# Kernel optimization log

Measured on AMD Instinct MI355X. Metric: run time of the kernel, lower is better.

Reference implementation:

```python
import jax, jax.numpy as jnp
import numpy as np

N_HEAD = 16

def setup_inputs() -> dict:
    key = jax.random.key(0)
    k1, k2, k3 = jax.random.split(key, 3)
    B, T, E = 4, 2048, 1024
    x = jax.random.normal(k1, (B, T, E), dtype=jnp.float32)
    w_attn = jax.random.normal(k2, (4 * E, E), dtype=jnp.float32) * (1.0 / np.sqrt(E))
    b_attn = jax.random.normal(k3, (4 * E,), dtype=jnp.float32) * 0.02
    return {"x": x, "w_attn": w_attn, "b_attn": b_attn}

def reference(x, w_attn, b_attn):
    B, T, C = x.shape
    H = N_HEAD
    D = C // H  # head_dim
    qkv = x @ w_attn.T + b_attn                      # [B,T,4C]
    q, k, v = qkv[..., :C], qkv[..., C:2*C], qkv[..., 2*C:3*C]  # 4th chunk unused
    q = q.reshape(B, T, H, D).transpose(0, 2, 1, 3)  # [B,H,T,D]
    k = k.reshape(B, T, H, D).transpose(0, 2, 1, 3)
    v = v.reshape(B, T, H, D).transpose(0, 2, 1, 3)
    scale = 1.0 / np.sqrt(D)
    attn = jnp.einsum('bhqd,bhkd->bhqk', q, k) * scale  # [B,H,T,T]
    causal = jnp.tril(jnp.ones((T, T), dtype=bool))
    attn = jnp.where(causal[None, None], attn, -jnp.inf)
    attn = jax.nn.softmax(attn, axis=-1)
    y = jnp.einsum('bhqk,bhkd->bhqd', attn, v)       # [B,H,T,D]
    return y.transpose(0, 2, 1, 3).reshape(B, T, C)
```

## Files before the change

kernel.cpp:

```cpp
#include <hip/hip_runtime.h>
#include <math.h>


using short8 = __attribute__((ext_vector_type(8))) short;
using f32x4  = __attribute__((ext_vector_type(4))) float;

__device__ __forceinline__ ushort f2bf(float f) {
    union { float f; unsigned u; } x{f};
    unsigned r = x.u + 0x7fffu + ((x.u >> 16) & 1u);
    return (ushort)(r >> 16);
}
__device__ __forceinline__ unsigned pack_bf16_ru(float a, float b) {
    union { float f; unsigned u; } x{a}, y{b};
    return __builtin_amdgcn_perm(y.u + 0x8000u, x.u + 0x8000u, 0x07060302u);
}

__device__ __forceinline__ void gload_lds16(const void* g, void* l) {
    __builtin_amdgcn_global_load_lds(
        (const __attribute__((address_space(1))) void*)g,
        (__attribute__((address_space(3))) void*)l, 16, 0, 0);
}

__global__ void cvt_all(const float* __restrict__ x, const float* __restrict__ w,
                        ushort* __restrict__ xb, ushort* __restrict__ wb) {
    int i = blockIdx.x * blockDim.x + threadIdx.x;
    const float* src; ushort* dst; int j;
    if (i < 2097152) { src = x; dst = xb; j = i; }
    else             { src = w; dst = wb; j = i - 2097152; if (j >= 786432) return; }
    float4 v = ((const float4*)src)[j];
    ushort4 o;
    o.x = f2bf(v.x); o.y = f2bf(v.y); o.z = f2bf(v.z); o.w = f2bf(v.w);
    ((ushort4*)dst)[j] = o;
}

__global__ __launch_bounds__(256) void qkv_gemm(
    const ushort* __restrict__ A, const ushort* __restrict__ W,
    const float* __restrict__ bias,
    ushort* __restrict__ Qo, ushort* __restrict__ Ko, ushort* __restrict__ Vt)
{
    __shared__ ushort As[128 * 64];
    __shared__ ushort Ws[128 * 64];
    const int id = (int)blockIdx.x;
    const int xcd = id & 7, s = id >> 3;
    const int bm = xcd * 8 + (s & 7);
    const int bn = s >> 3;
    const int tid = threadIdx.x;
    const int wave = tid >> 6, lane = tid & 63;
    const int quad = lane >> 4, l16 = lane & 15, l7 = l16 & 7;
    const int wm = (wave >> 1) * 64, wn = (wave & 1) * 64;

    const ushort* Abase = A + (size_t)(bm * 128) * 1024;
    const ushort* Wbase = W + (size_t)(bn * 128) * 1024;

    f32x4 acc[4][4];
#pragma unroll
    for (int i = 0; i < 4; i++)
#pragma unroll
        for (int j = 0; j < 4; j++) acc[i][j] = (f32x4){0.f, 0.f, 0.f, 0.f};

    for (int k0 = 0; k0 < 1024; k0 += 64) {
        __syncthreads();
#pragma unroll
        for (int j = 0; j < 4; j++) {
            const int rb = wave * 32 + j * 8;
            const int r  = rb + (lane >> 3);
            const int cc = (lane & 7) ^ (r & 7);
            gload_lds16(Abase + (size_t)r * 1024 + k0 + cc * 8, &As[rb * 64]);
            gload_lds16(Wbase + (size_t)r * 1024 + k0 + cc * 8, &Ws[rb * 64]);
        }
        __syncthreads();
        short8 af[4][2], wf[4][2];
#pragma unroll
        for (int t = 0; t < 4; t++)
#pragma unroll
            for (int kg = 0; kg < 2; kg++) {
                const int pc = ((kg * 4 + quad) ^ l7) * 8;
                af[t][kg] = *(const short8*)&As[(wm + t * 16 + l16) * 64 + pc];
                wf[t][kg] = *(const short8*)&Ws[(wn + t * 16 + l16) * 64 + pc];
            }
#pragma unroll
        for (int kg = 0; kg < 2; kg++)
#pragma unroll
            for (int tm = 0; tm < 4; tm++)
#pragma unroll
                for (int tn = 0; tn < 4; tn++)
                    acc[tm][tn] = __builtin_amdgcn_mfma_f32_16x16x32_bf16(af[tm][kg], wf[tn][kg], acc[tm][tn], 0, 0, 0);
    }

    const float SCALE_Q = 0.125f * 1.4426950408889634f;
#pragma unroll
    for (int tn = 0; tn < 4; tn++) {
        const int n = bn * 128 + wn + tn * 16 + l16;
        const float bv = bias[n];
#pragma unroll
        for (int tm = 0; tm < 4; tm++) {
            const int m0 = bm * 128 + wm + tm * 16 + quad * 4;
            const int b0 = m0 >> 11, t0 = m0 & 2047;
            if (n < 1024) {
                const int h = n >> 6, d = n & 63;
#pragma unroll
                for (int r = 0; r < 4; r++)
                    Qo[((size_t)(b0 * 16 + h) * 2048 + t0 + r) * 64 + d] = f2bf((acc[tm][tn][r] + bv) * SCALE_Q);
            } else if (n < 2048) {
                const int c = n - 1024, h = c >> 6, d = c & 63;
#pragma unroll
                for (int r = 0; r < 4; r++)
                    Ko[((size_t)(b0 * 16 + h) * 2048 + t0 + r) * 64 + d] = f2bf(acc[tm][tn][r] + bv);
            } else {
                const int c = n - 2048, h = c >> 6, d = c & 63;
                uint2 pk;
                pk.x = pack_bf16_ru(acc[tm][tn][0] + bv, acc[tm][tn][1] + bv);
                pk.y = pack_bf16_ru(acc[tm][tn][2] + bv, acc[tm][tn][3] + bv);
                *(uint2*)&Vt[((size_t)(b0 * 16 + h) * 64 + d) * 2048 + t0] = pk;
            }
        }
    }
}

__global__ __launch_bounds__(256) void attn_fwd(
    const ushort* __restrict__ Q, const ushort* __restrict__ K,
    const ushort* __restrict__ Vt, float* __restrict__ out)
{
    __shared__ ushort Ks[2][64 * 64];
    __shared__ ushort Vs[2][64 * 64];
    __shared__ ushort Ps[4][16 * 64];
    const int id = (int)blockIdx.x;
    const int bh = id & 63;
    const int s  = id >> 6;
    const int g = s >> 2, r4 = s & 3;
    const int qt = (g == 0) ? 15 - r4 : (g == 1) ? 8 + r4 : (g == 2) ? 7 - r4 : r4;
    const int b = bh >> 4, h = bh & 15;
    const int wave = threadIdx.x >> 6, lane = threadIdx.x & 63;
    const int quad = lane >> 4, l16 = lane & 15, l7 = l16 & 7;

    const ushort* Kbh = K  + (size_t)bh * 2048 * 64;
    const ushort* Vbh = Vt + (size_t)bh * 64 * 2048;
    ushort* Pw = Ps[wave];

    int qb[2];
    qb[0] = qt * 128 + wave * 16;
    qb[1] = qb[0] + 64;

    short8 qf[2][2];
#pragma unroll
    for (int qg = 0; qg < 2; qg++) {
        const ushort* Qp = Q + ((size_t)bh * 2048 + qb[qg] + l16) * 64;
        qf[qg][0] = *(const short8*)(Qp + quad * 8);
        qf[qg][1] = *(const short8*)(Qp + 32 + quad * 8);
    }

    f32x4 o[2][4];
#pragma unroll
    for (int qg = 0; qg < 2; qg++)
#pragma unroll
        for (int dg = 0; dg < 4; dg++) o[qg][dg] = (f32x4){0.f, 0.f, 0.f, 0.f};
    float lsum[2] = {0.f, 0.f};

    const int ntiles = 2 * qt + 2;

#define STAGE(k0_, bf_)                                                              \
    {                                                                                \
        _Pragma("unroll")                                                            \
        for (int j = 0; j < 2; j++) {                                                \
            const int rb = wave * 16 + j * 8;                                        \
            const int r  = rb + (lane >> 3);                                         \
            const int cc = (lane & 7) ^ (r & 7);                                     \
            gload_lds16(Kbh + (size_t)((k0_) + r) * 64 + cc * 8, &Ks[bf_][rb * 64]); \
            gload_lds16(Vbh + (size_t)r * 2048 + (k0_) + cc * 8, &Vs[bf_][rb * 64]); \
        }                                                                            \
    }

    STAGE(0, 0);
    int buf = 0, k0 = 0;
    for (int it = 0; it < ntiles; ++it, k0 += 64, buf ^= 1) {
        __syncthreads();
        if (it + 1 < ntiles) STAGE(k0 + 64, buf ^ 1);
        if (k0 > qb[1] + 15) continue;

        const bool act0 = k0 <= qb[0] + 15;

        short8 kf[4][2];
#pragma unroll
        for (int t = 0; t < 4; t++)
#pragma unroll
            for (int dh = 0; dh < 2; dh++)
                kf[t][dh] = *(const short8*)&Ks[buf][(t * 16 + l16) * 64 + (((dh * 4 + quad) ^ l7) * 8)];
        short8 vf[2][4];
#pragma unroll
        for (int kg = 0; kg < 2; kg++) {
            const int pc = ((kg * 4 + quad) ^ l7) * 8;
#pragma unroll
            for (int dg = 0; dg < 4; dg++)
                vf[kg][dg] = *(const short8*)&Vs[buf][(dg * 16 + l16) * 64 + pc];
        }

#pragma unroll
        for (int qg = 0; qg < 2; qg++) {
            if (qg == 0 && !act0) continue;
            f32x4 sc[4];
#pragma unroll
            for (int t = 0; t < 4; t++) {
                f32x4 z = (f32x4){0.f, 0.f, 0.f, 0.f};
                z = __builtin_amdgcn_mfma_f32_16x16x32_bf16(kf[t][0], qf[qg][0], z, 0, 0, 0);
                z = __builtin_amdgcn_mfma_f32_16x16x32_bf16(kf[t][1], qf[qg][1], z, 0, 0, 0);
                sc[t] = z;
            }
            const int q = qb[qg] + l16;
            float p[16], ps = 0.f;
            if (k0 + 63 > qb[qg]) {
#pragma unroll
                for (int t = 0; t < 4; t++)
#pragma unroll
                    for (int r = 0; r < 4; r++) {
                        const int key = k0 + t * 16 + quad * 4 + r;
                        const float sv = (key <= q) ? sc[t][r] : -INFINITY;
                        p[t * 4 + r] = __builtin_amdgcn_exp2f(sv);
                    }
            } else {
#pragma unroll
                for (int t = 0; t < 4; t++)
#pragma unroll
                    for (int r = 0; r < 4; r++)
                        p[t * 4 + r] = __builtin_amdgcn_exp2f(sc[t][r]);
            }
#pragma unroll
            for (int i = 0; i < 16; i++) ps += p[i];
            lsum[qg] += ps;
#pragma unroll
            for (int t = 0; t < 4; t++) {
                uint2 pk;
                pk.x = pack_bf16_ru(p[t * 4 + 0], p[t * 4 + 1]);
                pk.y = pack_bf16_ru(p[t * 4 + 2], p[t * 4 + 3]);
                const int pc = ((2 * t + (quad >> 1)) ^ l7) * 8 + (quad & 1) * 4;
                *(uint2*)(Pw + l16 * 64 + pc) = pk;
            }
#pragma unroll
            for (int kg = 0; kg < 2; kg++) {
                short8 pf = *(const short8*)(Pw + l16 * 64 + (((kg * 4 + quad) ^ l7) * 8));
#pragma unroll
                for (int dg = 0; dg < 4; dg++)
                    o[qg][dg] = __builtin_amdgcn_mfma_f32_16x16x32_bf16(vf[kg][dg], pf, o[qg][dg], 0, 0, 0);
            }
        }
    }
#undef STAGE

#pragma unroll
    for (int qg = 0; qg < 2; qg++) {
        float l = lsum[qg];
        l += __shfl_xor(l, 16);
        l += __shfl_xor(l, 32);
        const float rinv = 1.f / l;
        float* op = out + ((size_t)(b * 2048 + qb[qg] + l16)) * 1024 + h * 64;
#pragma unroll
        for (int dg = 0; dg < 4; dg++) {
            float4 v;
            v.x = o[qg][dg][0] * rinv; v.y = o[qg][dg][1] * rinv;
            v.z = o[qg][dg][2] * rinv; v.w = o[qg][dg][3] * rinv;
            *(float4*)(op + dg * 16 + quad * 4) = v;
        }
    }
}

extern "C" void kernel_launch(void* const* d_in, const int* in_sizes, int n_in,
                              void* d_out, int out_size, void* d_ws, size_t ws_size,
                              hipStream_t stream) {
    const float* x    = (const float*)d_in[0];
    const float* w    = (const float*)d_in[1];
    const float* bias = (const float*)d_in[2];

    ushort* xb  = (ushort*)d_ws;
    ushort* wb  = xb + 8388608;
    ushort* Qb  = wb + 3145728;
    ushort* Kb  = Qb + 8388608;
    ushort* Vtb = Kb + 8388608;

    cvt_all<<<11264, 256, 0, stream>>>(x, w, xb, wb);
    qkv_gemm<<<1536, 256, 0, stream>>>(xb, wb, bias, Qb, Kb, Vtb);
    attn_fwd<<<1024, 256, 0, stream>>>(Qb, Kb, Vtb, (float*)d_out);
}
```

Baseline: 219.9 us.

## Double-buffer QKV GEMM with 256x192 tiles and interleaved load/MFMA phases

Rewrites the QKV projection GEMM to use 512-thread blocks computing 256x192 output tiles, with double-buffered LDS. Global-to-LDS loads for the next K slice are issued in pieces between six MFMA phases, gated by explicit vmcnt waits and barriers, and MFMA priority is raised. The aim is to hide load latency and increase data reuse per block. In exchange it uses much more LDS and more registers per wave, reduces the number of blocks and occupancy, and depends on hand-tuned wait counts for correctness.

```diff
diff --git a/kernel.cpp b/kernel.cpp
--- a/kernel.cpp
+++ b/kernel.cpp
@@ -33,84 +33,129 @@
     ((ushort4*)dst)[j] = o;
 }
 
-__global__ __launch_bounds__(256) void qkv_gemm(
+__global__ __launch_bounds__(512) void qkv_gemm(
     const ushort* __restrict__ A, const ushort* __restrict__ W,
     const float* __restrict__ bias,
     ushort* __restrict__ Qo, ushort* __restrict__ Ko, ushort* __restrict__ Vt)
 {
-    __shared__ ushort As[128 * 64];
-    __shared__ ushort Ws[128 * 64];
+    __shared__ ushort As[2][256 * 64];
+    __shared__ ushort Ws[2][192 * 64];
     const int id = (int)blockIdx.x;
     const int xcd = id & 7, s = id >> 3;
-    const int bm = xcd * 8 + (s & 7);
-    const int bn = s >> 3;
+    const int bm = xcd * 4 + (s & 3);
+    const int bn = s >> 2;
     const int tid = threadIdx.x;
     const int wave = tid >> 6, lane = tid & 63;
     const int quad = lane >> 4, l16 = lane & 15, l7 = l16 & 7;
-    const int wm = (wave >> 1) * 64, wn = (wave & 1) * 64;
-
-    const ushort* Abase = A + (size_t)(bm * 128) * 1024;
-    const ushort* Wbase = W + (size_t)(bn * 128) * 1024;
-
-    f32x4 acc[4][4];
-#pragma unroll
-    for (int i = 0; i < 4; i++)
-#pragma unroll
-        for (int j = 0; j < 4; j++) acc[i][j] = (f32x4){0.f, 0.f, 0.f, 0.f};
-
-    for (int k0 = 0; k0 < 1024; k0 += 64) {
-        __syncthreads();
-#pragma unroll
-        for (int j = 0; j < 4; j++) {
-            const int rb = wave * 32 + j * 8;
-            const int r  = rb + (lane >> 3);
-            const int cc = (lane & 7) ^ (r & 7);
-            gload_lds16(Abase + (size_t)r * 1024 + k0 + cc * 8, &As[rb * 64]);
-            gload_lds16(Wbase + (size_t)r * 1024 + k0 + cc * 8, &Ws[rb * 64]);
-        }
-        __syncthreads();
-        short8 af[4][2], wf[4][2];
-#pragma unroll
-        for (int t = 0; t < 4; t++)
-#pragma unroll
-            for (int kg = 0; kg < 2; kg++) {
-                const int pc = ((kg * 4 + quad) ^ l7) * 8;
-                af[t][kg] = *(const short8*)&As[(wm + t * 16 + l16) * 64 + pc];
-                wf[t][kg] = *(const short8*)&Ws[(wn + t * 16 + l16) * 64 + pc];
-            }
-#pragma unroll
-        for (int kg = 0; kg < 2; kg++)
-#pragma unroll
-            for (int tm = 0; tm < 4; tm++)
-#pragma unroll
-                for (int tn = 0; tn < 4; tn++)
-                    acc[tm][tn] = __builtin_amdgcn_mfma_f32_16x16x32_bf16(af[tm][kg], wf[tn][kg], acc[tm][tn], 0, 0, 0);
-    }
+    const int wr = wave >> 2, wc = wave & 3;
+
+    const ushort* Abase = A + (size_t)(bm * 256) * 1024;
+    const ushort* Wbase = W + (size_t)(bn * 192) * 1024;
+
+    f32x4 acc[8][3];
+#pragma unroll
+    for (int i = 0; i < 8; i++)
+#pragma unroll
+        for (int j = 0; j < 3; j++) acc[i][j] = (f32x4){0.f, 0.f, 0.f, 0.f};
+
+#define STAGE_A(BB, H, KC)                                                          \
+    {                                                                               \
+        _Pragma("unroll")                                                           \
+        for (int j = 0; j < 2; j++) {                                               \
+            const int rb = (H) * 128 + j * 64 + wave * 8;                           \
+            const int r  = rb + (lane >> 3);                                        \
+            const int cc = (lane & 7) ^ ((lane >> 3) & 7);                          \
+            gload_lds16(Abase + (size_t)r * 1024 + (KC) + cc * 8, &As[BB][rb * 64]); \
+        }                                                                           \
+    }
+#define STAGE_W(BB, S3, KC)                                                         \
+    {                                                                               \
+        const int rb = (S3) * 64 + wave * 8;                                        \
+        const int r  = rb + (lane >> 3);                                            \
+        const int cc = (lane & 7) ^ ((lane >> 3) & 7);                              \
+        gload_lds16(Wbase + (size_t)r * 1024 + (KC) + cc * 8, &Ws[BB][rb * 64]);    \
+    }
+
+#define PHASE(BB, MS, NS)                                                           \
+    {                                                                               \
+        short8 af[4][2], wf[2];                                                     \
+        _Pragma("unroll")                                                           \
+        for (int mf = 0; mf < 4; mf++)                                              \
+            _Pragma("unroll")                                                       \
+            for (int kk = 0; kk < 2; kk++)                                          \
+                af[mf][kk] = *(const short8*)&As[BB][((MS) * 128 + wr * 64 + mf * 16 + l16) * 64 + (((kk * 4 + quad) ^ l7) * 8)]; \
+        _Pragma("unroll")                                                           \
+        for (int kk = 0; kk < 2; kk++)                                              \
+            wf[kk] = *(const short8*)&Ws[BB][((NS) * 64 + wc * 16 + l16) * 64 + (((kk * 4 + quad) ^ l7) * 8)]; \
+        __builtin_amdgcn_s_setprio(1);                                              \
+        _Pragma("unroll")                                                           \
+        for (int kk = 0; kk < 2; kk++)                                              \
+            _Pragma("unroll")                                                       \
+            for (int mf = 0; mf < 4; mf++)                                          \
+                acc[(MS) * 4 + mf][NS] = __builtin_amdgcn_mfma_f32_16x16x32_bf16(   \
+                    af[mf][kk], wf[kk], acc[(MS) * 4 + mf][NS], 0, 0, 0);           \
+        __builtin_amdgcn_s_setprio(0);                                              \
+    }
+
+#define VM(N)  asm volatile("s_waitcnt vmcnt(" #N ")" ::: "memory")
+#define BAR    asm volatile("s_barrier" ::: "memory")
+
+    STAGE_A(0, 0, 0);
+    STAGE_W(0, 0, 0);
+    STAGE_W(0, 1, 0);
+    STAGE_W(0, 2, 0);
+    STAGE_A(0, 1, 0);
+
+    int buf = 0;
+    for (int t = 0; t < 15; ++t, buf ^= 1) {
+        const int kn = (t + 1) * 64;
+        STAGE_A(buf ^ 1, 0, kn); VM(6); BAR; PHASE(buf, 0, 0);
+        STAGE_W(buf ^ 1, 0, kn); VM(6); BAR; PHASE(buf, 0, 1);
+        STAGE_W(buf ^ 1, 1, kn); VM(6); BAR; PHASE(buf, 0, 2);
+        STAGE_W(buf ^ 1, 2, kn); VM(5); BAR; PHASE(buf, 1, 0);
+        STAGE_A(buf ^ 1, 1, kn);        BAR; PHASE(buf, 1, 1);
+                                        BAR; PHASE(buf, 1, 2);
+    }
+    VM(4); BAR; PHASE(1, 0, 0);
+    VM(3); BAR; PHASE(1, 0, 1);
+    VM(2); BAR; PHASE(1, 0, 2);
+    VM(0); BAR; PHASE(1, 1, 0);
+                PHASE(1, 1, 1);
+                PHASE(1, 1, 2);
+
+#undef STAGE_A
+#undef STAGE_W
+#undef PHASE
+#undef VM
+#undef BAR
 
     const float SCALE_Q = 0.125f * 1.4426950408889634f;
 #pragma unroll
-    for (int tn = 0; tn < 4; tn++) {
-        const int n = bn * 128 + wn + tn * 16 + l16;
-        const float bv = bias[n];
-#pragma unroll
-        for (int tm = 0; tm < 4; tm++) {
-            const int m0 = bm * 128 + wm + tm * 16 + quad * 4;
-            const int b0 = m0 >> 11, t0 = m0 & 2047;
+    for (int ms = 0; ms < 2; ms++)
+#pragma unroll
+    for (int mf = 0; mf < 4; mf++) {
+        const int m0 = bm * 256 + ms * 128 + wr * 64 + mf * 16 + quad * 4;
+        const int b0 = m0 >> 11, t0 = m0 & 2047;
+#pragma unroll
+        for (int ns = 0; ns < 3; ns++) {
+            const int n = bn * 192 + ns * 64 + wc * 16 + l16;
+            const float bv = bias[n];
+            const f32x4 a = acc[ms * 4 + mf][ns];
             if (n < 1024) {
                 const int h = n >> 6, d = n & 63;
 #pragma unroll
                 for (int r = 0; r < 4; r++)
-                    Qo[((size_t)(b0 * 16 + h) * 2048 + t0 + r) * 64 + d] = f2bf((acc[tm][tn][r] + bv) * SCALE_Q);
+                    Qo[((size_t)(b0 * 16 + h) * 2048 + t0 + r) * 64 + d] = f2bf((a[r] + bv) * SCALE_Q);
             } else if (n < 2048) {
                 const int c = n - 1024, h = c >> 6, d = c & 63;
 #pragma unroll
                 for (int r = 0; r < 4; r++)
-                    Ko[((size_t)(b0 * 16 + h) * 2048 + t0 + r) * 64 + d] = f2bf(acc[tm][tn][r] + bv);
+                    Ko[((size_t)(b0 * 16 + h) * 2048 + t0 + r) * 64 + d] = f2bf(a[r] + bv);
             } else {
                 const int c = n - 2048, h = c >> 6, d = c & 63;
                 uint2 pk;
-                pk.x = pack_bf16_ru(acc[tm][tn][0] + bv, acc[tm][tn][1] + bv);
-                pk.y = pack_bf16_ru(acc[tm][tn][2] + bv, acc[tm][tn][3] + bv);
+                pk.x = pack_bf16_ru(a[0] + bv, a[1] + bv);
+                pk.y = pack_bf16_ru(a[2] + bv, a[3] + bv);
                 *(uint2*)&Vt[((size_t)(b0 * 16 + h) * 64 + d) * 2048 + t0] = pk;
             }
         }
@@ -276,6 +321,6 @@
     ushort* Vtb = Kb + 8388608;
 
     cvt_all<<<11264, 256, 0, stream>>>(x, w, xb, wb);
-    qkv_gemm<<<1536, 256, 0, stream>>>(xb, wb, bias, Qb, Kb, Vtb);
+    qkv_gemm<<<512, 512, 0, stream>>>(xb, wb, bias, Qb, Kb, Vtb);
     attn_fwd<<<1024, 256, 0, stream>>>(Qb, Kb, Vtb, (float*)d_out);
 }
```

Result: slower. 239.3 us (+8.8%).

## Interleave QK and softmax of both query groups, drop per-wave tile skipping

Applied to the files above, without the earlier changes.

The attention inner loop is restructured so the second query group's QK MFMAs are issued while the first group's softmax runs. The first group's P write, P reload and PV MFMAs are likewise staggered against the second group's softmax. The per-wave early-continue and the active-group check are removed, and causal masking is applied unconditionally on every tile. The aim is more instruction-level overlap between MFMA and VALU/LDS work with branch-free code. The cost is some fully masked tiles that now do redundant MFMA and exp work for waves whose rows lie before those keys.

```diff
diff --git a/kernel.cpp b/kernel.cpp
--- a/kernel.cpp
+++ b/kernel.cpp
@@ -157,6 +157,7 @@
     float lsum[2] = {0.f, 0.f};
 
     const int ntiles = 2 * qt + 2;
+    const int q0 = qb[0] + l16, q1 = qb[1] + l16;
 
 #define STAGE(k0_, bf_)                                                              \
     {                                                                                \
@@ -170,14 +171,43 @@
         }                                                                            \
     }
 
+#define SOFTMAX(SC, QV, LQ, PK)                                                      \
+    {                                                                                \
+        float p[16];                                                                 \
+        _Pragma("unroll")                                                            \
+        for (int t = 0; t < 4; t++)                                                  \
+            _Pragma("unroll")                                                        \
+            for (int r = 0; r < 4; r++) {                                            \
+                const int key = k0 + t * 16 + quad * 4 + r;                          \
+                const float sv = (key <= (QV)) ? SC[t][r] : -INFINITY;               \
+                p[t * 4 + r] = __builtin_amdgcn_exp2f(sv);                           \
+            }                                                                        \
+        const float s0_ = (p[0] + p[1]) + (p[2] + p[3]);                             \
+        const float s1_ = (p[4] + p[5]) + (p[6] + p[7]);                             \
+        const float s2_ = (p[8] + p[9]) + (p[10] + p[11]);                           \
+        const float s3_ = (p[12] + p[13]) + (p[14] + p[15]);                         \
+        (LQ) += (s0_ + s1_) + (s2_ + s3_);                                           \
+        _Pragma("unroll")                                                            \
+        for (int t = 0; t < 4; t++) {                                                \
+            PK[t].x = pack_bf16_ru(p[t * 4 + 0], p[t * 4 + 1]);                      \
+            PK[t].y = pack_bf16_ru(p[t * 4 + 2], p[t * 4 + 3]);                      \
+        }                                                                            \
+    }
+
+#define PWRITE(PK)                                                                   \
+    {                                                                                \
+        _Pragma("unroll")                                                            \
+        for (int t = 0; t < 4; t++) {                                                \
+            const int pc = ((2 * t + (quad >> 1)) ^ l7) * 8 + (quad & 1) * 4;        \
+            *(uint2*)(Pw + l16 * 64 + pc) = PK[t];                                   \
+        }                                                                            \
+    }
+
     STAGE(0, 0);
     int buf = 0, k0 = 0;
     for (int it = 0; it < ntiles; ++it, k0 += 64, buf ^= 1) {
         __syncthreads();
         if (it + 1 < ntiles) STAGE(k0 + 64, buf ^ 1);
-        if (k0 > qb[1] + 15) continue;
-
-        const bool act0 = k0 <= qb[0] + 15;
 
         short8 kf[4][2];
 #pragma unroll
@@ -185,6 +215,35 @@
 #pragma unroll
             for (int dh = 0; dh < 2; dh++)
                 kf[t][dh] = *(const short8*)&Ks[buf][(t * 16 + l16) * 64 + (((dh * 4 + quad) ^ l7) * 8)];
+
+        f32x4 sc0[4];
+#pragma unroll
+        for (int t = 0; t < 4; t++) {
+            f32x4 z = (f32x4){0.f, 0.f, 0.f, 0.f};
+            z = __builtin_amdgcn_mfma_f32_16x16x32_bf16(kf[t][0], qf[0][0], z, 0, 0, 0);
+            z = __builtin_amdgcn_mfma_f32_16x16x32_bf16(kf[t][1], qf[0][1], z, 0, 0, 0);
+            sc0[t] = z;
+        }
+        uint2 pk0[4];
+        SOFTMAX(sc0, q0, lsum[0], pk0);
+
+        f32x4 sc1[4];
+#pragma unroll
+        for (int t = 0; t < 4; t++) {
+            f32x4 z = (f32x4){0.f, 0.f, 0.f, 0.f};
+            z = __builtin_amdgcn_mfma_f32_16x16x32_bf16(kf[t][0], qf[1][0], z, 0, 0, 0);
+            z = __builtin_amdgcn_mfma_f32_16x16x32_bf16(kf[t][1], qf[1][1], z, 0, 0, 0);
+            sc1[t] = z;
+        }
+
+        PWRITE(pk0);
+        uint2 pk1[4];
+        SOFTMAX(sc1, q1, lsum[1], pk1);
+
+        short8 pf0[2];
+#pragma unroll
+        for (int kg = 0; kg < 2; kg++)
+            pf0[kg] = *(const short8*)(Pw + l16 * 64 + (((kg * 4 + quad) ^ l7) * 8));
         short8 vf[2][4];
 #pragma unroll
         for (int kg = 0; kg < 2; kg++) {
@@ -195,55 +254,25 @@
         }
 
 #pragma unroll
-        for (int qg = 0; qg < 2; qg++) {
-            if (qg == 0 && !act0) continue;
-            f32x4 sc[4];
-#pragma unroll
-            for (int t = 0; t < 4; t++) {
-                f32x4 z = (f32x4){0.f, 0.f, 0.f, 0.f};
-                z = __builtin_amdgcn_mfma_f32_16x16x32_bf16(kf[t][0], qf[qg][0], z, 0, 0, 0);
-                z = __builtin_amdgcn_mfma_f32_16x16x32_bf16(kf[t][1], qf[qg][1], z, 0, 0, 0);
-                sc[t] = z;
-            }
-            const int q = qb[qg] + l16;
-            float p[16], ps = 0.f;
-            if (k0 + 63 > qb[qg]) {
-#pragma unroll
-                for (int t = 0; t < 4; t++)
-#pragma unroll
-                    for (int r = 0; r < 4; r++) {
-                        const int key = k0 + t * 16 + quad * 4 + r;
-                        const float sv = (key <= q) ? sc[t][r] : -INFINITY;
-                        p[t * 4 + r] = __builtin_amdgcn_exp2f(sv);
-                    }
-            } else {
-#pragma unroll
-                for (int t = 0; t < 4; t++)
-#pragma unroll
-                    for (int r = 0; r < 4; r++)
-                        p[t * 4 + r] = __builtin_amdgcn_exp2f(sc[t][r]);
-            }
-#pragma unroll
-            for (int i = 0; i < 16; i++) ps += p[i];
-            lsum[qg] += ps;
-#pragma unroll
-            for (int t = 0; t < 4; t++) {
-                uint2 pk;
-                pk.x = pack_bf16_ru(p[t * 4 + 0], p[t * 4 + 1]);
-                pk.y = pack_bf16_ru(p[t * 4 + 2], p[t * 4 + 3]);
-                const int pc = ((2 * t + (quad >> 1)) ^ l7) * 8 + (quad & 1) * 4;
-                *(uint2*)(Pw + l16 * 64 + pc) = pk;
-            }
-#pragma unroll
-            for (int kg = 0; kg < 2; kg++) {
-                short8 pf = *(const short8*)(Pw + l16 * 64 + (((kg * 4 + quad) ^ l7) * 8));
-#pragma unroll
-                for (int dg = 0; dg < 4; dg++)
-                    o[qg][dg] = __builtin_amdgcn_mfma_f32_16x16x32_bf16(vf[kg][dg], pf, o[qg][dg], 0, 0, 0);
-            }
-        }
+        for (int kg = 0; kg < 2; kg++)
+#pragma unroll
+            for (int dg = 0; dg < 4; dg++)
+                o[0][dg] = __builtin_amdgcn_mfma_f32_16x16x32_bf16(vf[kg][dg], pf0[kg], o[0][dg], 0, 0, 0);
+
+        PWRITE(pk1);
+        short8 pf1[2];
+#pragma unroll
+        for (int kg = 0; kg < 2; kg++)
+            pf1[kg] = *(const short8*)(Pw + l16 * 64 + (((kg * 4 + quad) ^ l7) * 8));
+#pragma unroll
+        for (int kg = 0; kg < 2; kg++)
+#pragma unroll
+            for (int dg = 0; dg < 4; dg++)
+                o[1][dg] = __builtin_amdgcn_mfma_f32_16x16x32_bf16(vf[kg][dg], pf1[kg], o[1][dg], 0, 0, 0);
     }
 #undef STAGE
+#undef SOFTMAX
+#undef PWRITE
 
 #pragma unroll
     for (int qg = 0; qg < 2; qg++) {
```

Measured after the change: 232.6 us. 5.8% more time.
